# Kernel optimization log

Hardware: AMD Instinct MI355X
Metric: run time of the kernel (lower is better)

Reference implementation:

```python
import jax, jax.numpy as jnp
import numpy as np

NB_HEAD = 16
SIZE_PER_HEAD = 64
D_MODEL = 1024
OUT_DIM = NB_HEAD * SIZE_PER_HEAD
BIG_NEG = 1e10


def setup_inputs() -> dict:
    key = jax.random.key(0)
    ks = jax.random.split(key, 6)
    B, L = 2, 2048
    q = jax.random.normal(ks[0], (B, L, D_MODEL), dtype=jnp.float32)
    k = jax.random.normal(ks[1], (B, L, D_MODEL), dtype=jnp.float32)
    v = jax.random.normal(ks[2], (B, L, D_MODEL), dtype=jnp.float32)
    v_mask = jnp.ones((B, L), dtype=jnp.float32)
    q_mask = jnp.ones((B, L), dtype=jnp.float32)
    # glorot_normal-ish init for the three projection kernels
    std = (2.0 / (D_MODEL + OUT_DIM)) ** 0.5
    q_kernel = jax.random.normal(ks[3], (D_MODEL, OUT_DIM), dtype=jnp.float32) * std
    k_kernel = jax.random.normal(ks[4], (D_MODEL, OUT_DIM), dtype=jnp.float32) * std
    v_kernel = jax.random.normal(ks[5], (D_MODEL, OUT_DIM), dtype=jnp.float32) * std
    return {"q": q, "k": k, "v": v, "v_mask": v_mask, "q_mask": q_mask,
            "q_kernel": q_kernel, "k_kernel": k_kernel, "v_kernel": v_kernel}


def reference(q, k, v, v_mask, q_mask, q_kernel, k_kernel, v_kernel):
    B, Lq, _ = q.shape
    Lk = k.shape[1]
    H, D = NB_HEAD, SIZE_PER_HEAD
    # projections -> [B, L, H, D]
    qw = (q @ q_kernel).reshape(B, Lq, H, D)
    kw = (k @ k_kernel).reshape(B, Lk, H, D)
    vw = (v @ v_kernel).reshape(B, Lk, H, D)
    # scaled dot-product scores [B, H, Lq, Lk]
    scores = jnp.einsum('bqhd,bkhd->bhqk', qw, kw) / jnp.sqrt(jnp.float32(D))
    # additive key mask (original permutes so mask broadcasts over key axis)
    scores = scores - (1.0 - v_mask)[:, None, None, :] * BIG_NEG
    a = jax.nn.softmax(scores, axis=-1)
    # weighted sum -> [B, Lq, H, D] -> [B, Lq, H*D]
    o = jnp.einsum('bhqk,bkhd->bqhd', a, vw).reshape(B, Lq, H * D)
    # multiplicative query mask on output
    o = o * q_mask[:, :, None]
    return o
```

## Files before the change

kernel.cpp:

```cpp
#include <hip/hip_runtime.h>
#include <hip/hip_bf16.h>

#define B_SZ 2
#define SEQ  2048
#define DM   1024
#define NH   16
#define HD   64

typedef __attribute__((ext_vector_type(8))) short bf16x8;
typedef __attribute__((ext_vector_type(4))) short bf16x4;
typedef __attribute__((ext_vector_type(4))) float f32x4;

__device__ __forceinline__ short f2b(float f) {
    __hip_bfloat16 h = __float2bfloat16(f);
    return *reinterpret_cast<short*>(&h);
}

__device__ __forceinline__ void async_copy16(void* lds, const void* g) {
    __builtin_amdgcn_global_load_lds(
        (const __attribute__((address_space(1))) void*)g,
        (__attribute__((address_space(3))) void*)lds, 16, 0, 0);
}

__global__ __launch_bounds__(256) void kCvt(
    const float* __restrict__ q, const float* __restrict__ k, const float* __restrict__ v,
    short* __restrict__ qb, short* __restrict__ kb, short* __restrict__ vb) {
    const float* src = blockIdx.z == 0 ? q : (blockIdx.z == 1 ? k : v);
    short*       dst = blockIdx.z == 0 ? qb : (blockIdx.z == 1 ? kb : vb);
    size_t i = ((size_t)blockIdx.x * 256 + threadIdx.x) * 8;
    float4 a0 = *reinterpret_cast<const float4*>(src + i);
    float4 a1 = *reinterpret_cast<const float4*>(src + i + 4);
    bf16x8 c;
    c[0] = f2b(a0.x); c[1] = f2b(a0.y); c[2] = f2b(a0.z); c[3] = f2b(a0.w);
    c[4] = f2b(a1.x); c[5] = f2b(a1.y); c[6] = f2b(a1.z); c[7] = f2b(a1.w);
    *reinterpret_cast<bf16x8*>(dst + i) = c;
}

__global__ __launch_bounds__(256) void kT(
    const float* __restrict__ w0, const float* __restrict__ w1, const float* __restrict__ w2,
    short* __restrict__ t0, short* __restrict__ t1, short* __restrict__ t2) {
    const float* w = blockIdx.z == 0 ? w0 : (blockIdx.z == 1 ? w1 : w2);
    short*       t = blockIdx.z == 0 ? t0 : (blockIdx.z == 1 ? t1 : t2);
    __shared__ float tile[64][65];
    int n0 = blockIdx.x * 64, k0 = blockIdx.y * 64;
    int tid = threadIdx.x;
    int c = tid & 63, rr = tid >> 6;
#pragma unroll
    for (int i = 0; i < 16; i++) {
        int kk = i * 4 + rr;
        tile[kk][c] = w[(size_t)(k0 + kk) * DM + n0 + c];
    }
    __syncthreads();
#pragma unroll
    for (int i = 0; i < 16; i++) {
        int nn = i * 4 + rr;
        t[(size_t)(n0 + nn) * DM + k0 + c] = f2b(tile[c][nn]);
    }
}

__global__ __launch_bounds__(256) void kProj(
    const short* __restrict__ qb, const short* __restrict__ kb, const short* __restrict__ vb,
    const short* __restrict__ wtq, const short* __restrict__ wtk, const short* __restrict__ wtv,
    short* __restrict__ qw, short* __restrict__ kw, short* __restrict__ vwT) {
    int z = blockIdx.z;
    const short* A  = z == 0 ? qb : (z == 1 ? kb : vb);
    const short* Bt = z == 0 ? wtq : (z == 1 ? wtk : wtv);

    __shared__ short As[128 * 64];
    __shared__ short Bs[128 * 64];

    int tid = threadIdx.x;
    int m0 = blockIdx.y * 128, n0 = blockIdx.x * 128;
    int wv = tid >> 6, lane = tid & 63, quad = lane >> 4, ln = lane & 15;
    int rblk = (wv >> 1) * 64, cblk = (wv & 1) * 64;

    int rA = wv * 32;
    int srow = rA + (lane >> 3), scol = (lane & 7) * 8;

    f32x4 zero = {0.f, 0.f, 0.f, 0.f};
    f32x4 acc[4][4];
#pragma unroll
    for (int rt = 0; rt < 4; rt++)
#pragma unroll
        for (int ct = 0; ct < 4; ct++) acc[rt][ct] = zero;

    for (int ks = 0; ks < DM; ks += 64) {
        const short* gA = A  + (size_t)(m0 + srow) * DM + ks + scol;
        const short* gB = Bt + (size_t)(n0 + srow) * DM + ks + scol;
#pragma unroll
        for (int i = 0; i < 4; i++) {
            async_copy16(&As[(rA + i * 8) * 64], gA + (size_t)i * 8 * DM);
            async_copy16(&Bs[(rA + i * 8) * 64], gB + (size_t)i * 8 * DM);
        }
        __syncthreads();
#pragma unroll
        for (int kc = 0; kc < 2; kc++) {
            bf16x8 af[4], bfv[4];
#pragma unroll
            for (int rt = 0; rt < 4; rt++)
                af[rt] = *reinterpret_cast<bf16x8*>(&As[(rblk + rt * 16 + ln) * 64 + kc * 32 + quad * 8]);
#pragma unroll
            for (int ct = 0; ct < 4; ct++)
                bfv[ct] = *reinterpret_cast<bf16x8*>(&Bs[(cblk + ct * 16 + ln) * 64 + kc * 32 + quad * 8]);
#pragma unroll
            for (int rt = 0; rt < 4; rt++)
#pragma unroll
                for (int ct = 0; ct < 4; ct++)
                    acc[rt][ct] = __builtin_amdgcn_mfma_f32_16x16x32_bf16(
                        af[rt], bfv[ct], acc[rt][ct], 0, 0, 0);
        }
        __syncthreads();
    }

    if (z < 2) {
        short* C = z == 0 ? qw : kw;
#pragma unroll
        for (int rt = 0; rt < 4; rt++)
#pragma unroll
            for (int r = 0; r < 4; r++) {
                int row = m0 + rblk + rt * 16 + quad * 4 + r;
#pragma unroll
                for (int ct = 0; ct < 4; ct++)
                    C[(size_t)row * DM + n0 + cblk + ct * 16 + ln] = f2b(acc[rt][ct][r]);
            }
    } else {
#pragma unroll
        for (int rt = 0; rt < 4; rt++) {
            int srow0 = m0 + rblk + rt * 16 + quad * 4;
            int bb = srow0 >> 11, lk = srow0 & (SEQ - 1);
#pragma unroll
            for (int ct = 0; ct < 4; ct++) {
                int coln = n0 + cblk + ct * 16 + ln;
                int hh = coln >> 6, dd = coln & 63;
                bf16x4 pk;
                pk[0] = f2b(acc[rt][ct][0]); pk[1] = f2b(acc[rt][ct][1]);
                pk[2] = f2b(acc[rt][ct][2]); pk[3] = f2b(acc[rt][ct][3]);
                *reinterpret_cast<bf16x4*>(
                    &vwT[(((size_t)bb * NH + hh) * HD + dd) * SEQ + lk]) = pk;
            }
        }
    }
}

__global__ __launch_bounds__(512) void kAttn(
    const short* __restrict__ qw, const short* __restrict__ kw, const short* __restrict__ vwT,
    const float* __restrict__ vmask, const float* __restrict__ qmask, float* __restrict__ out) {
    int b = blockIdx.z, h = blockIdx.y, lq0 = blockIdx.x * 128;
    int tid = threadIdx.x, wv = tid >> 6, lane = tid & 63, quad = lane >> 4, ln = lane & 15;

    __shared__ short Ks[64][72];
    __shared__ short Vt[64][72];
    __shared__ short Ps[8][16][72];

    const short* qrow = qw + (size_t)(b * SEQ + lq0 + wv * 16 + ln) * DM + h * HD;
    bf16x8 qf0 = *reinterpret_cast<const bf16x8*>(qrow + quad * 8);
    bf16x8 qf1 = *reinterpret_cast<const bf16x8*>(qrow + 32 + quad * 8);

    f32x4 zero = {0.f, 0.f, 0.f, 0.f};
    float mrow = -1e30f, lrow = 0.f;
    f32x4 o[4];
#pragma unroll
    for (int dt = 0; dt < 4; dt++) o[dt] = zero;

    int sr = tid >> 3, sc = (tid & 7) * 8;
    const float* vmb = vmask + b * SEQ;

    for (int lk0 = 0; lk0 < SEQ; lk0 += 64) {
        {
            const short* kp = kw + (size_t)(b * SEQ + lk0 + sr) * DM + h * HD + sc;
            *reinterpret_cast<bf16x8*>(&Ks[sr][sc]) = *reinterpret_cast<const bf16x8*>(kp);
            const short* vp = vwT + ((size_t)(b * NH + h) * HD + sr) * SEQ + lk0 + sc;
            *reinterpret_cast<bf16x8*>(&Vt[sr][sc]) = *reinterpret_cast<const bf16x8*>(vp);
        }
        __syncthreads();

        f32x4 s[4];
#pragma unroll
        for (int lt = 0; lt < 4; lt++) s[lt] = zero;
#pragma unroll
        for (int lt = 0; lt < 4; lt++) {
            bf16x8 kf0 = *reinterpret_cast<bf16x8*>(&Ks[lt * 16 + ln][quad * 8]);
            bf16x8 kf1 = *reinterpret_cast<bf16x8*>(&Ks[lt * 16 + ln][32 + quad * 8]);
            s[lt] = __builtin_amdgcn_mfma_f32_16x16x32_bf16(kf0, qf0, s[lt], 0, 0, 0);
            s[lt] = __builtin_amdgcn_mfma_f32_16x16x32_bf16(kf1, qf1, s[lt], 0, 0, 0);
        }

#pragma unroll
        for (int lt = 0; lt < 4; lt++) {
            float4 mv = *reinterpret_cast<const float4*>(&vmb[lk0 + lt * 16 + quad * 4]);
            s[lt][0] = s[lt][0] * 0.125f - (1.0f - mv.x) * 1e10f;
            s[lt][1] = s[lt][1] * 0.125f - (1.0f - mv.y) * 1e10f;
            s[lt][2] = s[lt][2] * 0.125f - (1.0f - mv.z) * 1e10f;
            s[lt][3] = s[lt][3] * 0.125f - (1.0f - mv.w) * 1e10f;
        }

        float mc = s[0][0];
#pragma unroll
        for (int lt = 0; lt < 4; lt++)
#pragma unroll
            for (int r = 0; r < 4; r++) mc = fmaxf(mc, s[lt][r]);
        mc = fmaxf(mc, __shfl_xor(mc, 16));
        mc = fmaxf(mc, __shfl_xor(mc, 32));

        float mn = fmaxf(mrow, mc);
        float alpha = __expf(mrow - mn);
        mrow = mn;

        float rs = 0.f;
#pragma unroll
        for (int lt = 0; lt < 4; lt++)
#pragma unroll
            for (int r = 0; r < 4; r++) {
                float p = __expf(s[lt][r] - mn);
                s[lt][r] = p;
                rs += p;
            }
        rs += __shfl_xor(rs, 16);
        rs += __shfl_xor(rs, 32);
        lrow = lrow * alpha + rs;

#pragma unroll
        for (int dt = 0; dt < 4; dt++)
#pragma unroll
            for (int r = 0; r < 4; r++) o[dt][r] *= alpha;

#pragma unroll
        for (int lt = 0; lt < 4; lt++)
#pragma unroll
            for (int r = 0; r < 4; r++)
                Ps[wv][ln][lt * 16 + quad * 4 + r] = f2b(s[lt][r]);

        bf16x8 pf0 = *reinterpret_cast<bf16x8*>(&Ps[wv][ln][quad * 8]);
        bf16x8 pf1 = *reinterpret_cast<bf16x8*>(&Ps[wv][ln][32 + quad * 8]);

#pragma unroll
        for (int dt = 0; dt < 4; dt++) {
            bf16x8 vf0 = *reinterpret_cast<bf16x8*>(&Vt[dt * 16 + ln][quad * 8]);
            bf16x8 vf1 = *reinterpret_cast<bf16x8*>(&Vt[dt * 16 + ln][32 + quad * 8]);
            o[dt] = __builtin_amdgcn_mfma_f32_16x16x32_bf16(vf0, pf0, o[dt], 0, 0, 0);
            o[dt] = __builtin_amdgcn_mfma_f32_16x16x32_bf16(vf1, pf1, o[dt], 0, 0, 0);
        }
        __syncthreads();
    }

    int lq = lq0 + wv * 16 + ln;
    float sc2 = (1.0f / lrow) * qmask[b * SEQ + lq];
#pragma unroll
    for (int dt = 0; dt < 4; dt++) {
        float4 st;
        st.x = o[dt][0] * sc2; st.y = o[dt][1] * sc2;
        st.z = o[dt][2] * sc2; st.w = o[dt][3] * sc2;
        *reinterpret_cast<float4*>(
            &out[(size_t)(b * SEQ + lq) * DM + h * HD + dt * 16 + quad * 4]) = st;
    }
}

extern "C" void kernel_launch(void* const* d_in, const int* in_sizes, int n_in,
                              void* d_out, int out_size, void* d_ws, size_t ws_size,
                              hipStream_t stream) {
    const float* q  = (const float*)d_in[0];
    const float* k  = (const float*)d_in[1];
    const float* v  = (const float*)d_in[2];
    const float* vm = (const float*)d_in[3];
    const float* qm = (const float*)d_in[4];
    const float* qk = (const float*)d_in[5];
    const float* kk = (const float*)d_in[6];
    const float* vk = (const float*)d_in[7];
    float* out = (float*)d_out;

    short* ws  = (short*)d_ws;
    short* wtq = ws;
    short* wtk = wtq + 1024 * 1024;
    short* wtv = wtk + 1024 * 1024;
    short* vb  = wtv + 1024 * 1024;
    short* qw  = vb + (size_t)4096 * 1024;
    short* kw  = qw + (size_t)4096 * 1024;
    short* vwT = kw + (size_t)4096 * 1024;
    short* qb = (short*)d_out;
    short* kb = qb + (size_t)4096 * 1024;

    kCvt <<<dim3(2048, 1, 3), 256, 0, stream>>>(q, k, v, qb, kb, vb);
    kT   <<<dim3(16, 16, 3), 256, 0, stream>>>(qk, kk, vk, wtq, wtk, wtv);
    kProj<<<dim3(8, 32, 3), 256, 0, stream>>>(qb, kb, vb, wtq, wtk, wtv, qw, kw, vwT);
    kAttn<<<dim3(16, 16, 2), 512, 0, stream>>>(qw, kw, vwT, vm, qm, out);
}
```

Measured before the change: 255.7 us.

## Merge preprocessing kernels and double-width KV tiles with register prefetch in attention

Merges the input conversion and weight transpose kernels into a single launch, where the weight-transpose z-slices exit early for most blocks. The attention kernel now processes 128 keys per iteration instead of 64 and prefetches the next K/V tile into registers while computing on the current one, halving the number of barriers. The P tile is written as packed 4-element stores. This raises LDS use and register pressure and launches 2048x3 blocks that return immediately.

Result: faster. 243.9 us (-4.6%).

```diff
diff --git a/kernel.cpp b/kernel.cpp
--- a/kernel.cpp
+++ b/kernel.cpp
@@ -22,39 +22,40 @@
         (__attribute__((address_space(3))) void*)lds, 16, 0, 0);
 }
 
-__global__ __launch_bounds__(256) void kCvt(
+__global__ __launch_bounds__(256) void kPre(
     const float* __restrict__ q, const float* __restrict__ k, const float* __restrict__ v,
-    short* __restrict__ qb, short* __restrict__ kb, short* __restrict__ vb) {
-    const float* src = blockIdx.z == 0 ? q : (blockIdx.z == 1 ? k : v);
-    short*       dst = blockIdx.z == 0 ? qb : (blockIdx.z == 1 ? kb : vb);
-    size_t i = ((size_t)blockIdx.x * 256 + threadIdx.x) * 8;
-    float4 a0 = *reinterpret_cast<const float4*>(src + i);
-    float4 a1 = *reinterpret_cast<const float4*>(src + i + 4);
-    bf16x8 c;
-    c[0] = f2b(a0.x); c[1] = f2b(a0.y); c[2] = f2b(a0.z); c[3] = f2b(a0.w);
-    c[4] = f2b(a1.x); c[5] = f2b(a1.y); c[6] = f2b(a1.z); c[7] = f2b(a1.w);
-    *reinterpret_cast<bf16x8*>(dst + i) = c;
-}
-
-__global__ __launch_bounds__(256) void kT(
     const float* __restrict__ w0, const float* __restrict__ w1, const float* __restrict__ w2,
+    short* __restrict__ qb, short* __restrict__ kb, short* __restrict__ vb,
     short* __restrict__ t0, short* __restrict__ t1, short* __restrict__ t2) {
-    const float* w = blockIdx.z == 0 ? w0 : (blockIdx.z == 1 ? w1 : w2);
-    short*       t = blockIdx.z == 0 ? t0 : (blockIdx.z == 1 ? t1 : t2);
-    __shared__ float tile[64][65];
-    int n0 = blockIdx.x * 64, k0 = blockIdx.y * 64;
-    int tid = threadIdx.x;
-    int c = tid & 63, rr = tid >> 6;
-#pragma unroll
-    for (int i = 0; i < 16; i++) {
-        int kk = i * 4 + rr;
-        tile[kk][c] = w[(size_t)(k0 + kk) * DM + n0 + c];
-    }
-    __syncthreads();
-#pragma unroll
-    for (int i = 0; i < 16; i++) {
-        int nn = i * 4 + rr;
-        t[(size_t)(n0 + nn) * DM + k0 + c] = f2b(tile[c][nn]);
+    int z = blockIdx.z, tid = threadIdx.x;
+    if (z < 3) {
+        const float* src = z == 0 ? q : (z == 1 ? k : v);
+        short*       dst = z == 0 ? qb : (z == 1 ? kb : vb);
+        size_t i = ((size_t)blockIdx.x * 256 + tid) * 8;
+        float4 a0 = *reinterpret_cast<const float4*>(src + i);
+        float4 a1 = *reinterpret_cast<const float4*>(src + i + 4);
+        bf16x8 c;
+        c[0] = f2b(a0.x); c[1] = f2b(a0.y); c[2] = f2b(a0.z); c[3] = f2b(a0.w);
+        c[4] = f2b(a1.x); c[5] = f2b(a1.y); c[6] = f2b(a1.z); c[7] = f2b(a1.w);
+        *reinterpret_cast<bf16x8*>(dst + i) = c;
+    } else {
+        if (blockIdx.x >= 256) return;
+        const float* w = z == 3 ? w0 : (z == 4 ? w1 : w2);
+        short*       t = z == 3 ? t0 : (z == 4 ? t1 : t2);
+        __shared__ float tile[64][65];
+        int n0 = (blockIdx.x & 15) * 64, k0 = (blockIdx.x >> 4) * 64;
+        int c = tid & 63, rr = tid >> 6;
+#pragma unroll
+        for (int i = 0; i < 16; i++) {
+            int kk = i * 4 + rr;
+            tile[kk][c] = w[(size_t)(k0 + kk) * DM + n0 + c];
+        }
+        __syncthreads();
+#pragma unroll
+        for (int i = 0; i < 16; i++) {
+            int nn = i * 4 + rr;
+            t[(size_t)(n0 + nn) * DM + k0 + c] = f2b(tile[c][nn]);
+        }
     }
 }
 
@@ -148,9 +149,9 @@
     int b = blockIdx.z, h = blockIdx.y, lq0 = blockIdx.x * 128;
     int tid = threadIdx.x, wv = tid >> 6, lane = tid & 63, quad = lane >> 4, ln = lane & 15;
 
-    __shared__ short Ks[64][72];
-    __shared__ short Vt[64][72];
-    __shared__ short Ps[8][16][72];
+    __shared__ short Ks[128][72];
+    __shared__ short Vt[64][136];
+    __shared__ short Ps[8][16][136];
 
     const short* qrow = qw + (size_t)(b * SEQ + lq0 + wv * 16 + ln) * DM + h * HD;
     bf16x8 qf0 = *reinterpret_cast<const bf16x8*>(qrow + quad * 8);
@@ -162,23 +163,39 @@
 #pragma unroll
     for (int dt = 0; dt < 4; dt++) o[dt] = zero;
 
-    int sr = tid >> 3, sc = (tid & 7) * 8;
+    int krow = tid >> 2, kcol = (tid & 3) * 16;
+    int vrow = tid >> 3, vcol = (tid & 7) * 16;
+    const short* kp = kw + (size_t)(b * SEQ + krow) * DM + h * HD + kcol;
+    const short* vp = vwT + ((size_t)(b * NH + h) * HD + vrow) * SEQ + vcol;
     const float* vmb = vmask + b * SEQ;
 
-    for (int lk0 = 0; lk0 < SEQ; lk0 += 64) {
-        {
-            const short* kp = kw + (size_t)(b * SEQ + lk0 + sr) * DM + h * HD + sc;
-            *reinterpret_cast<bf16x8*>(&Ks[sr][sc]) = *reinterpret_cast<const bf16x8*>(kp);
-            const short* vp = vwT + ((size_t)(b * NH + h) * HD + sr) * SEQ + lk0 + sc;
-            *reinterpret_cast<bf16x8*>(&Vt[sr][sc]) = *reinterpret_cast<const bf16x8*>(vp);
-        }
-        __syncthreads();
-
-        f32x4 s[4];
-#pragma unroll
-        for (int lt = 0; lt < 4; lt++) s[lt] = zero;
-#pragma unroll
-        for (int lt = 0; lt < 4; lt++) {
+    bf16x8 kr0 = *reinterpret_cast<const bf16x8*>(kp);
+    bf16x8 kr1 = *reinterpret_cast<const bf16x8*>(kp + 8);
+    bf16x8 vr0 = *reinterpret_cast<const bf16x8*>(vp);
+    bf16x8 vr1 = *reinterpret_cast<const bf16x8*>(vp + 8);
+
+    for (int it = 0; it < SEQ / 128; it++) {
+        int lk0 = it * 128;
+        *reinterpret_cast<bf16x8*>(&Ks[krow][kcol])     = kr0;
+        *reinterpret_cast<bf16x8*>(&Ks[krow][kcol + 8]) = kr1;
+        *reinterpret_cast<bf16x8*>(&Vt[vrow][vcol])     = vr0;
+        *reinterpret_cast<bf16x8*>(&Vt[vrow][vcol + 8]) = vr1;
+        __syncthreads();
+
+        if (it + 1 < SEQ / 128) {
+            kp += (size_t)128 * DM;
+            vp += 128;
+            kr0 = *reinterpret_cast<const bf16x8*>(kp);
+            kr1 = *reinterpret_cast<const bf16x8*>(kp + 8);
+            vr0 = *reinterpret_cast<const bf16x8*>(vp);
+            vr1 = *reinterpret_cast<const bf16x8*>(vp + 8);
+        }
+
+        f32x4 s[8];
+#pragma unroll
+        for (int lt = 0; lt < 8; lt++) s[lt] = zero;
+#pragma unroll
+        for (int lt = 0; lt < 8; lt++) {
             bf16x8 kf0 = *reinterpret_cast<bf16x8*>(&Ks[lt * 16 + ln][quad * 8]);
             bf16x8 kf1 = *reinterpret_cast<bf16x8*>(&Ks[lt * 16 + ln][32 + quad * 8]);
             s[lt] = __builtin_amdgcn_mfma_f32_16x16x32_bf16(kf0, qf0, s[lt], 0, 0, 0);
@@ -186,7 +203,7 @@
         }
 
 #pragma unroll
-        for (int lt = 0; lt < 4; lt++) {
+        for (int lt = 0; lt < 8; lt++) {
             float4 mv = *reinterpret_cast<const float4*>(&vmb[lk0 + lt * 16 + quad * 4]);
             s[lt][0] = s[lt][0] * 0.125f - (1.0f - mv.x) * 1e10f;
             s[lt][1] = s[lt][1] * 0.125f - (1.0f - mv.y) * 1e10f;
@@ -196,7 +213,7 @@
 
         float mc = s[0][0];
 #pragma unroll
-        for (int lt = 0; lt < 4; lt++)
+        for (int lt = 0; lt < 8; lt++)
 #pragma unroll
             for (int r = 0; r < 4; r++) mc = fmaxf(mc, s[lt][r]);
         mc = fmaxf(mc, __shfl_xor(mc, 16));
@@ -208,7 +225,7 @@
 
         float rs = 0.f;
 #pragma unroll
-        for (int lt = 0; lt < 4; lt++)
+        for (int lt = 0; lt < 8; lt++)
 #pragma unroll
             for (int r = 0; r < 4; r++) {
                 float p = __expf(s[lt][r] - mn);
@@ -225,21 +242,25 @@
             for (int r = 0; r < 4; r++) o[dt][r] *= alpha;
 
 #pragma unroll
-        for (int lt = 0; lt < 4; lt++)
-#pragma unroll
-            for (int r = 0; r < 4; r++)
-                Ps[wv][ln][lt * 16 + quad * 4 + r] = f2b(s[lt][r]);
-
-        bf16x8 pf0 = *reinterpret_cast<bf16x8*>(&Ps[wv][ln][quad * 8]);
-        bf16x8 pf1 = *reinterpret_cast<bf16x8*>(&Ps[wv][ln][32 + quad * 8]);
-
-#pragma unroll
-        for (int dt = 0; dt < 4; dt++) {
-            bf16x8 vf0 = *reinterpret_cast<bf16x8*>(&Vt[dt * 16 + ln][quad * 8]);
-            bf16x8 vf1 = *reinterpret_cast<bf16x8*>(&Vt[dt * 16 + ln][32 + quad * 8]);
-            o[dt] = __builtin_amdgcn_mfma_f32_16x16x32_bf16(vf0, pf0, o[dt], 0, 0, 0);
-            o[dt] = __builtin_amdgcn_mfma_f32_16x16x32_bf16(vf1, pf1, o[dt], 0, 0, 0);
-        }
+        for (int lt = 0; lt < 8; lt++) {
+            bf16x4 pk;
+            pk[0] = f2b(s[lt][0]); pk[1] = f2b(s[lt][1]);
+            pk[2] = f2b(s[lt][2]); pk[3] = f2b(s[lt][3]);
+            *reinterpret_cast<bf16x4*>(&Ps[wv][ln][lt * 16 + quad * 4]) = pk;
+        }
+
+        bf16x8 pf[4];
+#pragma unroll
+        for (int kk = 0; kk < 4; kk++)
+            pf[kk] = *reinterpret_cast<bf16x8*>(&Ps[wv][ln][kk * 32 + quad * 8]);
+
+#pragma unroll
+        for (int dt = 0; dt < 4; dt++)
+#pragma unroll
+            for (int kk = 0; kk < 4; kk++) {
+                bf16x8 vf = *reinterpret_cast<bf16x8*>(&Vt[dt * 16 + ln][kk * 32 + quad * 8]);
+                o[dt] = __builtin_amdgcn_mfma_f32_16x16x32_bf16(vf, pf[kk], o[dt], 0, 0, 0);
+            }
         __syncthreads();
     }
 
@@ -279,8 +300,8 @@
     short* qb = (short*)d_out;
     short* kb = qb + (size_t)4096 * 1024;
 
-    kCvt <<<dim3(2048, 1, 3), 256, 0, stream>>>(q, k, v, qb, kb, vb);
-    kT   <<<dim3(16, 16, 3), 256, 0, stream>>>(qk, kk, vk, wtq, wtk, wtv);
+    kPre <<<dim3(2048, 1, 6), 256, 0, stream>>>(q, k, v, qk, kk, vk,
+                                                qb, kb, vb, wtq, wtk, wtv);
     kProj<<<dim3(8, 32, 3), 256, 0, stream>>>(qb, kb, vb, wtq, wtk, wtv, qw, kw, vwT);
     kAttn<<<dim3(16, 16, 2), 512, 0, stream>>>(qw, kw, vwT, vm, qm, out);
 }
```
